# Kernel tuning notes

Measured on AMD Instinct MI355X. Metric: run time of the kernel, lower is better.

## Reference

```python
import jax, jax.numpy as jnp
import numpy as np

C = 128      # channels
ALPHA = 0.5
B, LX, LY = 8, 128, 1024


def setup_inputs() -> dict:
    key = jax.random.key(0)
    ks = jax.random.split(key, 10)
    s = 1.0 / np.sqrt(C)
    sh = 1.0 / np.sqrt(C // 2)
    return {
        "x": jax.random.normal(ks[0], (B, C, LX), dtype=jnp.float32),
        "y": jax.random.normal(ks[1], (B, C, LY), dtype=jnp.float32),
        "W_drug": jax.random.uniform(ks[2], (C, C), jnp.float32, -s, s),
        "b_drug": jax.random.uniform(ks[3], (C,), jnp.float32, -s, s),
        "W_prot": jax.random.uniform(ks[4], (C, C), jnp.float32, -s, s),
        "b_prot": jax.random.uniform(ks[5], (C,), jnp.float32, -s, s),
        "W_down": jax.random.uniform(ks[6], (C, C // 2), jnp.float32, -s, s),
        "b_down": jax.random.uniform(ks[7], (C // 2,), jnp.float32, -s, s),
        "W_up": jax.random.uniform(ks[8], (C // 2, C), jnp.float32, -sh, sh),
        "b_up": jax.random.uniform(ks[9], (C,), jnp.float32, -sh, sh),
    }


def reference(x, y, W_drug, b_drug, W_prot, b_prot, W_down, b_down, W_up, b_up):
    # x: [B, C, Lx], y: [B, C, Ly]
    drug_att = jnp.einsum("bcl,cd->bld", x, W_drug) + b_drug      # [B, Lx, C]
    prot_att = jnp.einsum("bcl,cd->bld", y, W_prot) + b_prot      # [B, Ly, C]
    # broadcast-add -> [B, Lx, Ly, C]
    s = jax.nn.relu(drug_att[:, :, None, :] + prot_att[:, None, :, :])
    h = jax.nn.relu(jnp.einsum("bxyc,ch->bxyh", s, W_down) + b_down)  # [B,Lx,Ly,C/2]
    atten = jnp.einsum("bxyh,hc->bxyc", h, W_up) + b_up              # [B,Lx,Ly,C]
    comp = jnp.mean(atten, axis=2)   # [B, Lx, C]
    prot = jnp.mean(atten, axis=1)   # [B, Ly, C]
    comp_g = comp.transpose(0, 2, 1)  # [B, C, Lx]
    prot_g = prot.transpose(0, 2, 1)  # [B, C, Ly]
    comp_gate = jax.nn.sigmoid(comp_g) * jnp.tanh(comp_g)
    prot_gate = jax.nn.sigmoid(prot_g) * jnp.tanh(prot_g)
    drug_out = x * ALPHA + x * comp_gate
    prot_out = y * ALPHA + y * prot_gate
    return (drug_out, prot_out)
```

## Files before the change

kernel.cpp:

```cpp
#include <hip/hip_runtime.h>
#include <hip/hip_bf16.h>
#include <math.h>

#define B_  8
#define C_  128
#define CH_ 64
#define LX_ 128
#define LY_ 1024

typedef __attribute__((ext_vector_type(8)))  _Float16 half8;
typedef __attribute__((ext_vector_type(16))) float f32x16;

__global__ __launch_bounds__(128) void k1_att(
    const float* __restrict__ x, const float* __restrict__ y,
    const float* __restrict__ Wd, const float* __restrict__ bd,
    const float* __restrict__ Wp, const float* __restrict__ bp,
    const float* __restrict__ Wdown,
    _Float16* __restrict__ datt, _Float16* __restrict__ patt,
    _Float16* __restrict__ wdTh)
{
    const int blk = blockIdx.x;
    const int t = threadIdx.x;
    if (blk < 64) {
        int u = blk * 128 + t;
        wdTh[u] = (_Float16)Wdown[(u & 127) * CH_ + (u >> 7)];
    }
    const float* src; const float* W; const float* bias; _Float16* dst; int L;
    int b, l0;
    if (blk < 256) {
        int row0 = blk * 4; b = row0 >> 7; l0 = row0 & 127;
        src = x; W = Wd; bias = bd; dst = datt; L = LX_;
    } else {
        int row0 = (blk - 256) * 4; b = row0 >> 10; l0 = row0 & 1023;
        src = y; W = Wp; bias = bp; dst = patt; L = LY_;
    }
    __shared__ float col[4][128];
    {
        const float* sp = src + ((long)b * C_ + t) * L + l0;
        float4 v = *(const float4*)sp;
        col[0][t] = v.x; col[1][t] = v.y; col[2][t] = v.z; col[3][t] = v.w;
    }
    __syncthreads();
    float acc0 = bias[t], acc1 = acc0, acc2 = acc0, acc3 = acc0;
    #pragma unroll 8
    for (int c = 0; c < 128; ++c) {
        float w = W[c * 128 + t];
        float s0 = col[0][c], s1 = col[1][c], s2 = col[2][c], s3 = col[3][c];
        acc0 = fmaf(s0, w, acc0); acc1 = fmaf(s1, w, acc1);
        acc2 = fmaf(s2, w, acc2); acc3 = fmaf(s3, w, acc3);
    }
    _Float16* dp = dst + ((long)b * L + l0) * C_ + t;
    dp[0]      = (_Float16)acc0; dp[C_]     = (_Float16)acc1;
    dp[2 * C_] = (_Float16)acc2; dp[3 * C_] = (_Float16)acc3;
}

__global__ __launch_bounds__(256, 2) void k2_main(
    const _Float16* __restrict__ datt, const _Float16* __restrict__ patt,
    const _Float16* __restrict__ wdTh, const float* __restrict__ bdown,
    float* __restrict__ HxP, float* __restrict__ HyP)
{
    const int b     = blockIdx.x >> 2;
    const int lxblk = blockIdx.x & 3;
    const int lyblk = blockIdx.y;
    const int t   = threadIdx.x;
    const int w   = t >> 6;
    const int l   = t & 63;
    const int h   = l >> 5;
    const int c32 = l & 31;

    __shared__ float compWp[32][2][66];
    __shared__ float protP[4][32][66];

    const _Float16* w0 = wdTh + c32 * C_ + h * 8;
    const _Float16* w1 = wdTh + (32 + c32) * C_ + h * 8;
    const _Float16* prow = patt + ((long)(b * LY_) + lyblk * 32 + c32) * C_ + h * 8;
    half8 bf0[8], bf1[8], pv[8];
    #pragma unroll
    for (int kt = 0; kt < 8; ++kt) {
        bf0[kt] = *(const half8*)(w0 + kt * 16);
        bf1[kt] = *(const half8*)(w1 + kt * 16);
        pv[kt]  = *(const half8*)(prow + kt * 16);
    }
    const float bdr0 = bdown[c32], bdr1 = bdown[32 + c32];

    const _Float16* dbase =
        datt + ((long)(b * LX_) + lxblk * 32 + w * 8) * C_ + h * 8;
    const half8 hz = {};
    float hy0[16], hy1[16];
    #pragma unroll
    for (int r = 0; r < 16; ++r) { hy0[r] = 0.f; hy1[r] = 0.f; }

    half8 dcA[8], dcB[8];
    #pragma unroll
    for (int kt = 0; kt < 8; ++kt)
        dcA[kt] = *(const half8*)(dbase + kt * 16);

#define K2_COMPUTE(ROW, DC)                                                   \
    {                                                                         \
        f32x16 acc0 = {}, acc1 = {};                                          \
        _Pragma("unroll")                                                     \
        for (int kt = 0; kt < 8; ++kt) {                                      \
            half8 s = __builtin_elementwise_max(DC[kt] + pv[kt], hz);         \
            acc0 = __builtin_amdgcn_mfma_f32_32x32x16_f16(s, bf0[kt], acc0, 0, 0, 0); \
            acc1 = __builtin_amdgcn_mfma_f32_32x32x16_f16(s, bf1[kt], acc1, 0, 0, 0); \
        }                                                                     \
        float s0 = 0.f, s1 = 0.f;                                             \
        _Pragma("unroll")                                                     \
        for (int r = 0; r < 16; ++r) {                                        \
            float va = fmaxf(acc0[r] + bdr0, 0.f);                            \
            float vb = fmaxf(acc1[r] + bdr1, 0.f);                            \
            hy0[r] += va; hy1[r] += vb;                                       \
            s0 += va; s1 += vb;                                               \
        }                                                                     \
        const int lxi = w * 8 + (ROW);                                        \
        compWp[lxi][h][c32]      = s0;                                        \
        compWp[lxi][h][32 + c32] = s1;                                        \
    }

    #pragma unroll 1
    for (int lxp = 0; lxp < 4; ++lxp) {
        const int rA = lxp * 2, rB = rA + 1;
        {
            const _Float16* dp = dbase + rB * C_;
            #pragma unroll
            for (int kt = 0; kt < 8; ++kt) dcB[kt] = *(const half8*)(dp + kt * 16);
        }
        K2_COMPUTE(rA, dcA);
        {
            const _Float16* dp = dbase + ((rB + 1) & 7) * C_;
            #pragma unroll
            for (int kt = 0; kt < 8; ++kt) dcA[kt] = *(const half8*)(dp + kt * 16);
        }
        K2_COMPUTE(rB, dcB);
    }
#undef K2_COMPUTE

    #pragma unroll
    for (int r = 0; r < 16; ++r) {
        int ly = (r & 3) + 8 * (r >> 2) + 4 * h;
        protP[w][ly][c32]      = hy0[r];
        protP[w][ly][32 + c32] = hy1[r];
    }
    __syncthreads();

    {
        float* hxp = HxP + ((long)lyblk * (B_ * LX_) + b * LX_ + lxblk * 32) * 64;
        float* hyp = HyP + ((long)lxblk * (B_ * LY_) + b * LY_ + lyblk * 32) * 64;
        for (int u = t; u < 2048; u += 256) {
            int r = u >> 6, c = u & 63;
            hxp[u] = compWp[r][0][c] + compWp[r][1][c];
            hyp[u] = (protP[0][r][c] + protP[1][r][c])
                   + (protP[2][r][c] + protP[3][r][c]);
        }
    }
}

__global__ __launch_bounds__(256) void k3_gate(
    const float* __restrict__ HxP, const float* __restrict__ HyP,
    const float* __restrict__ wup, const float* __restrict__ bup,
    const float* __restrict__ x, const float* __restrict__ y,
    float* __restrict__ out)
{
    const int b = blockIdx.y;
    const int t = threadIdx.x;
    const float* part; const float* xin; float* outp; int L; float invN; int l0;
    int nq; long qstr;
    if (blockIdx.x < 4) {
        part = HxP; nq = 32; qstr = (long)B_ * LX_ * 64;
        xin = x; outp = out; L = LX_; invN = 1.f / 1024.f; l0 = blockIdx.x * 32;
    } else {
        part = HyP; nq = 4;  qstr = (long)B_ * LY_ * 64;
        xin = y; outp = out + (long)B_ * C_ * LX_; L = LY_; invN = 1.f / 128.f;
        l0 = (blockIdx.x - 4) * 32;
    }
    __shared__ float Ht[32][72];
    __shared__ float Wt[64][136];
    __shared__ float gg[32][133];

    const float* p0 = part + ((long)b * L + l0) * 64;
    for (int u = t; u < 2048; u += 256) {
        float a0 = 0.f, a1 = 0.f, a2 = 0.f, a3 = 0.f;
        #pragma unroll 4
        for (int q = 0; q < nq; q += 4) {
            a0 += p0[(long)q * qstr + u];
            a1 += p0[(long)(q + 1) * qstr + u];
            a2 += p0[(long)(q + 2) * qstr + u];
            a3 += p0[(long)(q + 3) * qstr + u];
        }
        Ht[u >> 6][u & 63] = (a0 + a1) + (a2 + a3);
    }
    #pragma unroll
    for (int i = 0; i < 8; ++i) {
        int idx = t + i * 256;
        int r = idx >> 5, c4 = (idx & 31) * 4;
        *(float4*)&Wt[r][c4] = *(const float4*)(wup + idx * 4);
    }
    __syncthreads();

    const int lrow = t >> 3, cg = (t & 7) * 4;
    float acc[4][4];
    #pragma unroll
    for (int jj = 0; jj < 4; ++jj)
        #pragma unroll
        for (int i = 0; i < 4; ++i) acc[jj][i] = 0.f;
    #pragma unroll 4
    for (int k = 0; k < 64; ++k) {
        float hv = Ht[lrow][k];
        #pragma unroll
        for (int jj = 0; jj < 4; ++jj) {
            float4 wv = *(const float4*)&Wt[k][cg + 32 * jj];
            acc[jj][0] = fmaf(hv, wv.x, acc[jj][0]);
            acc[jj][1] = fmaf(hv, wv.y, acc[jj][1]);
            acc[jj][2] = fmaf(hv, wv.z, acc[jj][2]);
            acc[jj][3] = fmaf(hv, wv.w, acc[jj][3]);
        }
    }
    #pragma unroll
    for (int jj = 0; jj < 4; ++jj)
        #pragma unroll
        for (int i = 0; i < 4; ++i) {
            int c = cg + 32 * jj + i;
            float v = fmaf(acc[jj][i], invN, bup[c]);
            float sg = 1.f / (1.f + expf(-v));
            gg[lrow][c] = sg * tanhf(v);
        }
    __syncthreads();
    for (int u = t; u < 4096; u += 256) {
        int c = u >> 5, li = u & 31;
        long idx = ((long)b * C_ + c) * L + l0 + li;
        outp[idx] = xin[idx] * (0.5f + gg[li][c]);
    }
}

extern "C" void kernel_launch(void* const* d_in, const int* in_sizes, int n_in,
                              void* d_out, int out_size, void* d_ws, size_t ws_size,
                              hipStream_t stream) {
    (void)in_sizes; (void)n_in; (void)out_size; (void)ws_size;
    const float* x     = (const float*)d_in[0];
    const float* y     = (const float*)d_in[1];
    const float* Wdrug = (const float*)d_in[2];
    const float* bdrug = (const float*)d_in[3];
    const float* Wprot = (const float*)d_in[4];
    const float* bprot = (const float*)d_in[5];
    const float* Wdown = (const float*)d_in[6];
    const float* bdown = (const float*)d_in[7];
    const float* Wup   = (const float*)d_in[8];
    const float* bup   = (const float*)d_in[9];
    float* out = (float*)d_out;
    char* ws = (char*)d_ws;

    _Float16* datt = (_Float16*)ws;
    _Float16* patt = (_Float16*)(ws + 262144);
    _Float16* wdTh = (_Float16*)(ws + 2359296);
    float*    HxP  = (float*)(ws + 2375680);
    float*    HyP  = (float*)(ws + 10764288);

    hipLaunchKernelGGL(k1_att, dim3(2304), dim3(128), 0, stream,
                       x, y, Wdrug, bdrug, Wprot, bprot, Wdown, datt, patt, wdTh);
    hipLaunchKernelGGL(k2_main, dim3(32, 32), dim3(256), 0, stream,
                       datt, patt, wdTh, bdown, HxP, HyP);
    hipLaunchKernelGGL(k3_gate, dim3(36, 8), dim3(256), 0, stream,
                       HxP, HyP, Wup, bup, x, y, out);
}
```

Baseline: 65.70 us.

## Software-pipeline MFMA compute with readout of previous row's accumulators

Restructures the per-row loop in the pair kernel so the MFMA chain for row i+1 is issued before the bias/ReLU/reduction readout of row i, using two alternating accumulator sets. It also collapses the double-buffered row registers into one buffer loaded right after each compute. The intent is to hide MFMA latency behind VALU readout work. The cost is more accumulator registers live at once (64 extra floats), which may lower occupancy or cause spills.

```diff
diff --git a/kernel.cpp b/kernel.cpp
--- a/kernel.cpp
+++ b/kernel.cpp
@@ -82,6 +82,7 @@
         pv[kt]  = *(const half8*)(prow + kt * 16);
     }
     const float bdr0 = bdown[c32], bdr1 = bdown[32 + c32];
+    const f32x16 zero16 = {};
 
     const _Float16* dbase =
         datt + ((long)(b * LX_) + lxblk * 32 + w * 8) * C_ + h * 8;
@@ -90,25 +91,40 @@
     #pragma unroll
     for (int r = 0; r < 16; ++r) { hy0[r] = 0.f; hy1[r] = 0.f; }
 
-    half8 dcA[8], dcB[8];
+    half8 dv[8];
     #pragma unroll
     for (int kt = 0; kt < 8; ++kt)
-        dcA[kt] = *(const half8*)(dbase + kt * 16);
-
-#define K2_COMPUTE(ROW, DC)                                                   \
+        dv[kt] = *(const half8*)(dbase + kt * 16);
+
+    f32x16 accA0, accA1, accB0, accB1;
+
+#define K2_COMPUTE(A0, A1)                                                    \
     {                                                                         \
-        f32x16 acc0 = {}, acc1 = {};                                          \
+        half8 s = __builtin_elementwise_max(dv[0] + pv[0], hz);               \
+        A0 = __builtin_amdgcn_mfma_f32_32x32x16_f16(s, bf0[0], zero16, 0, 0, 0); \
+        A1 = __builtin_amdgcn_mfma_f32_32x32x16_f16(s, bf1[0], zero16, 0, 0, 0); \
         _Pragma("unroll")                                                     \
-        for (int kt = 0; kt < 8; ++kt) {                                      \
-            half8 s = __builtin_elementwise_max(DC[kt] + pv[kt], hz);         \
-            acc0 = __builtin_amdgcn_mfma_f32_32x32x16_f16(s, bf0[kt], acc0, 0, 0, 0); \
-            acc1 = __builtin_amdgcn_mfma_f32_32x32x16_f16(s, bf1[kt], acc1, 0, 0, 0); \
+        for (int kt = 1; kt < 8; ++kt) {                                      \
+            half8 s2 = __builtin_elementwise_max(dv[kt] + pv[kt], hz);        \
+            A0 = __builtin_amdgcn_mfma_f32_32x32x16_f16(s2, bf0[kt], A0, 0, 0, 0); \
+            A1 = __builtin_amdgcn_mfma_f32_32x32x16_f16(s2, bf1[kt], A1, 0, 0, 0); \
         }                                                                     \
+    }
+
+#define K2_LOAD(ROW)                                                          \
+    {                                                                         \
+        const _Float16* dp_ = dbase + (ROW) * C_;                             \
+        _Pragma("unroll")                                                     \
+        for (int kt = 0; kt < 8; ++kt) dv[kt] = *(const half8*)(dp_ + kt * 16); \
+    }
+
+#define K2_READOUT(A0, A1, ROW)                                               \
+    {                                                                         \
         float s0 = 0.f, s1 = 0.f;                                             \
         _Pragma("unroll")                                                     \
         for (int r = 0; r < 16; ++r) {                                        \
-            float va = fmaxf(acc0[r] + bdr0, 0.f);                            \
-            float vb = fmaxf(acc1[r] + bdr1, 0.f);                            \
+            float va = fmaxf(A0[r] + bdr0, 0.f);                              \
+            float vb = fmaxf(A1[r] + bdr1, 0.f);                              \
             hy0[r] += va; hy1[r] += vb;                                       \
             s0 += va; s1 += vb;                                               \
         }                                                                     \
@@ -117,23 +133,24 @@
         compWp[lxi][h][32 + c32] = s1;                                        \
     }
 
+    K2_COMPUTE(accA0, accA1)
+    K2_LOAD(1)
     #pragma unroll 1
-    for (int lxp = 0; lxp < 4; ++lxp) {
-        const int rA = lxp * 2, rB = rA + 1;
-        {
-            const _Float16* dp = dbase + rB * C_;
-            #pragma unroll
-            for (int kt = 0; kt < 8; ++kt) dcB[kt] = *(const half8*)(dp + kt * 16);
-        }
-        K2_COMPUTE(rA, dcA);
-        {
-            const _Float16* dp = dbase + ((rB + 1) & 7) * C_;
-            #pragma unroll
-            for (int kt = 0; kt < 8; ++kt) dcA[kt] = *(const half8*)(dp + kt * 16);
-        }
-        K2_COMPUTE(rB, dcB);
-    }
+    for (int p = 0; p < 3; ++p) {
+        const int rB = 2 * p + 1, rA = 2 * p + 2;
+        K2_COMPUTE(accB0, accB1)
+        K2_LOAD(rB + 1)
+        K2_READOUT(accA0, accA1, rB - 1)
+        K2_COMPUTE(accA0, accA1)
+        K2_LOAD(rA + 1)
+        K2_READOUT(accB0, accB1, rA - 1)
+    }
+    K2_COMPUTE(accB0, accB1)
+    K2_READOUT(accA0, accA1, 6)
+    K2_READOUT(accB0, accB1, 7)
 #undef K2_COMPUTE
+#undef K2_LOAD
+#undef K2_READOUT
 
     #pragma unroll
     for (int r = 0; r < 16; ++r) {
```

New measurement: 80.89 us. +23.1%, slower.

## Split k2 into single-wave blocks over 16 Lx rows with XCD-aware block swizzle

Applied to the files above, without the earlier changes.

k2_main now launches 2048 single-wavefront blocks, each handling 16 Lx rows against 32 Ly rows, in place of 1024 four-wave blocks of 32x32. The cross-wave shared-memory reduction for the Ly partials goes away: each wave writes its Hy partials straight to global memory, and k3 now sums 8 Lx-group partials instead of 4. A block-index swizzle (raw&7)*256 spreads consecutive blocks across XCDs. The aim is more parallelism and fewer syncs and less LDS traffic, at the cost of doubled HyP partial traffic and a longer serial loop per wave.

```diff
diff --git a/kernel.cpp b/kernel.cpp
--- a/kernel.cpp
+++ b/kernel.cpp
@@ -54,22 +54,21 @@
     dp[2 * C_] = (_Float16)acc2; dp[3 * C_] = (_Float16)acc3;
 }
 
-__global__ __launch_bounds__(256, 2) void k2_main(
+__global__ __launch_bounds__(64, 2) void k2_main(
     const _Float16* __restrict__ datt, const _Float16* __restrict__ patt,
     const _Float16* __restrict__ wdTh, const float* __restrict__ bdown,
     float* __restrict__ HxP, float* __restrict__ HyP)
 {
-    const int b     = blockIdx.x >> 2;
-    const int lxblk = blockIdx.x & 3;
-    const int lyblk = blockIdx.y;
-    const int t   = threadIdx.x;
-    const int w   = t >> 6;
-    const int l   = t & 63;
+    const int raw = blockIdx.x;
+    const int bid = (raw & 7) * 256 + (raw >> 3);
+    const int lyblk = bid & 31;
+    const int lxg   = (bid >> 5) & 7;
+    const int b     = bid >> 8;
+    const int l   = threadIdx.x;
     const int h   = l >> 5;
     const int c32 = l & 31;
 
-    __shared__ float compWp[32][2][66];
-    __shared__ float protP[4][32][66];
+    __shared__ float HxL[16][2][64];
 
     const _Float16* w0 = wdTh + c32 * C_ + h * 8;
     const _Float16* w1 = wdTh + (32 + c32) * C_ + h * 8;
@@ -82,10 +81,10 @@
         pv[kt]  = *(const half8*)(prow + kt * 16);
     }
     const float bdr0 = bdown[c32], bdr1 = bdown[32 + c32];
-
+    const half8 hz = {};
     const _Float16* dbase =
-        datt + ((long)(b * LX_) + lxblk * 32 + w * 8) * C_ + h * 8;
-    const half8 hz = {};
+        datt + ((long)(b * LX_) + lxg * 16) * C_ + h * 8;
+
     float hy0[16], hy1[16];
     #pragma unroll
     for (int r = 0; r < 16; ++r) { hy0[r] = 0.f; hy1[r] = 0.f; }
@@ -112,45 +111,46 @@
             hy0[r] += va; hy1[r] += vb;                                       \
             s0 += va; s1 += vb;                                               \
         }                                                                     \
-        const int lxi = w * 8 + (ROW);                                        \
-        compWp[lxi][h][c32]      = s0;                                        \
-        compWp[lxi][h][32 + c32] = s1;                                        \
+        HxL[ROW][h][c32]      = s0;                                           \
+        HxL[ROW][h][32 + c32] = s1;                                           \
+    }
+
+#define K2_LOAD(ROW, DC)                                                      \
+    {                                                                         \
+        const _Float16* dp_ = dbase + ((ROW) & 15) * C_;                      \
+        _Pragma("unroll")                                                     \
+        for (int kt = 0; kt < 8; ++kt) DC[kt] = *(const half8*)(dp_ + kt * 16); \
     }
 
     #pragma unroll 1
-    for (int lxp = 0; lxp < 4; ++lxp) {
-        const int rA = lxp * 2, rB = rA + 1;
-        {
-            const _Float16* dp = dbase + rB * C_;
-            #pragma unroll
-            for (int kt = 0; kt < 8; ++kt) dcB[kt] = *(const half8*)(dp + kt * 16);
-        }
-        K2_COMPUTE(rA, dcA);
-        {
-            const _Float16* dp = dbase + ((rB + 1) & 7) * C_;
-            #pragma unroll
-            for (int kt = 0; kt < 8; ++kt) dcA[kt] = *(const half8*)(dp + kt * 16);
-        }
-        K2_COMPUTE(rB, dcB);
+    for (int p = 0; p < 8; ++p) {
+        const int rA = 2 * p, rB = 2 * p + 1;
+        K2_LOAD(rB, dcB)
+        K2_COMPUTE(rA, dcA)
+        K2_LOAD(rB + 1, dcA)
+        K2_COMPUTE(rB, dcB)
     }
 #undef K2_COMPUTE
-
-    #pragma unroll
-    for (int r = 0; r < 16; ++r) {
-        int ly = (r & 3) + 8 * (r >> 2) + 4 * h;
-        protP[w][ly][c32]      = hy0[r];
-        protP[w][ly][32 + c32] = hy1[r];
-    }
-    __syncthreads();
+#undef K2_LOAD
 
     {
-        float* hxp = HxP + ((long)lyblk * (B_ * LX_) + b * LX_ + lxblk * 32) * 64;
-        float* hyp = HyP + ((long)lxblk * (B_ * LY_) + b * LY_ + lyblk * 32) * 64;
-        for (int u = t; u < 2048; u += 256) {
-            int r = u >> 6, c = u & 63;
-            hxp[u] = compWp[r][0][c] + compWp[r][1][c];
-            hyp[u] = (protP[0][r][c] + protP[1][r][c])
-                   + (protP[2][r][c] + protP[3][r][c]);
+        float* hyp = HyP + (((long)lxg * B_ + b) * LY_ + lyblk * 32) * 64;
+        #pragma unroll
+        for (int rr = 0; rr < 16; ++rr) {
+            int ly = (rr & 3) + 8 * (rr >> 2) + 4 * h;
+            hyp[(long)ly * 64 + c32]      = hy0[rr];
+            hyp[(long)ly * 64 + 32 + c32] = hy1[rr];
+        }
+    }
+    __syncthreads();
+
+    {
+        float* hxp = HxP + (((long)lyblk * B_ + b) * LX_ + lxg * 16) * 64;
+        #pragma unroll
+        for (int i = 0; i < 16; ++i) {
+            int u = l + i * 64;
+            int r = u >> 6, kh = u & 63;
+            hxp[u] = HxL[r][0][kh] + HxL[r][1][kh];
         }
     }
 }
@@ -169,7 +169,7 @@
         part = HxP; nq = 32; qstr = (long)B_ * LX_ * 64;
         xin = x; outp = out; L = LX_; invN = 1.f / 1024.f; l0 = blockIdx.x * 32;
     } else {
-        part = HyP; nq = 4;  qstr = (long)B_ * LY_ * 64;
+        part = HyP; nq = 8;  qstr = (long)B_ * LY_ * 64;
         xin = y; outp = out + (long)B_ * C_ * LX_; L = LY_; invN = 1.f / 128.f;
         l0 = (blockIdx.x - 4) * 32;
     }
@@ -257,7 +257,7 @@
 
     hipLaunchKernelGGL(k1_att, dim3(2304), dim3(128), 0, stream,
                        x, y, Wdrug, bdrug, Wprot, bprot, Wdown, datt, patt, wdTh);
-    hipLaunchKernelGGL(k2_main, dim3(32, 32), dim3(256), 0, stream,
+    hipLaunchKernelGGL(k2_main, dim3(2048), dim3(64), 0, stream,
                        datt, patt, wdTh, bdown, HxP, HyP);
     hipLaunchKernelGGL(k3_gate, dim3(36, 8), dim3(256), 0, stream,
                        HxP, HyP, Wup, bup, x, y, out);
```

After: 66.53 us. No clear change (+1.3%).
